# Kernel tuning notes

Measured on AMD Instinct MI355X. Metric: run time of the kernel, lower is better.

## Reference

```python
import jax, jax.numpy as jnp
import numpy as np

B, L, DIM, H, HD = 1, 2048, 2048, 16, 128  # head_dim = DIM // H; RoPE pairs = HD // 2


def setup_inputs() -> dict:
    key = jax.random.key(0)
    ks = jax.random.split(key, 6)
    x = jax.random.normal(ks[0], (B, L, DIM), dtype=jnp.float32)
    pe = jax.random.normal(ks[1], (1, 1, L, HD // 2, 2, 2), dtype=jnp.float32)
    qkv_w = jax.random.normal(ks[2], (3 * DIM, DIM), dtype=jnp.float32) * 0.02
    q_scale = jnp.ones((HD,), dtype=jnp.float32)
    k_scale = jnp.ones((HD,), dtype=jnp.float32)
    proj_w = jax.random.normal(ks[3], (DIM, DIM), dtype=jnp.float32) * 0.02
    proj_b = jnp.zeros((DIM,), dtype=jnp.float32)
    return {"x": x, "pe": pe, "qkv_w": qkv_w, "q_scale": q_scale,
            "k_scale": k_scale, "proj_w": proj_w, "proj_b": proj_b}


def _rmsnorm(t, scale):
    # per-head-dim RMSNorm, eps=1e-6, computed in fp32 (inputs already fp32)
    rrms = jax.lax.rsqrt(jnp.mean(t * t, axis=-1, keepdims=True) + 1e-6)
    return t * rrms * scale


def _apply_rope(q, k, pe):
    def rot(t):
        t_ = t.reshape(*t.shape[:-1], -1, 1, 2)  # [B,H,L,HD/2,1,2]
        out = pe[..., 0] * t_[..., 0] + pe[..., 1] * t_[..., 1]  # [B,H,L,HD/2,2]
        return out.reshape(t.shape)
    return rot(q), rot(k)


def reference(x, pe, qkv_w, q_scale, k_scale, proj_w, proj_b):
    b, l, _ = x.shape
    qkv = jnp.einsum('bld,ed->ble', x, qkv_w)  # [B, L, 3*DIM]
    qkv = qkv.reshape(b, l, 3, H, HD)
    # 'B L (K H D) -> K B H L D'
    qkv = jnp.transpose(qkv, (2, 0, 3, 1, 4))
    q, k, v = qkv[0], qkv[1], qkv[2]  # each [B, H, L, HD]
    q = _rmsnorm(q, q_scale)
    k = _rmsnorm(k, k_scale)
    q, k = _apply_rope(q, k, pe)
    scale = 1.0 / jnp.sqrt(jnp.asarray(HD, dtype=q.dtype))
    scores = jnp.einsum('bhqd,bhkd->bhqk', q, k) * scale
    attn = jax.nn.softmax(scores, axis=-1)
    out = jnp.einsum('bhqk,bhkd->bhqd', attn, v)  # [B, H, L, HD]
    out = jnp.transpose(out, (0, 2, 1, 3)).reshape(b, l, H * HD)  # 'B H L D -> B L (H D)'
    return jnp.einsum('bld,ed->ble', out, proj_w) + proj_b
```

## Files before the change

kernel.cpp:

```cpp
#include <hip/hip_runtime.h>
#include <hip/hip_bf16.h>
#include <math.h>

#define L_SEQ 2048
#define DIM   2048
#define NH    16
#define HD    128
#define TDIM  6144

typedef __attribute__((ext_vector_type(8))) short short8;
typedef __attribute__((ext_vector_type(4))) float f32x4;
typedef __attribute__((ext_vector_type(16))) float f32x16;
typedef __attribute__((ext_vector_type(4))) unsigned int u32x4;

__device__ __forceinline__ void gl_lds16(const void* g, void* l) {
  __builtin_amdgcn_global_load_lds(
      (const __attribute__((address_space(1))) unsigned int*)g,
      (__attribute__((address_space(3))) unsigned int*)l, 16, 0, 0);
}

__device__ __forceinline__ short bf16bits(float x) {
  __hip_bfloat16 h = __float2bfloat16(x);
  return *(short*)&h;
}

__device__ __forceinline__ float bits2f(short s) {
  unsigned int u = ((unsigned int)(unsigned short)s) << 16;
  return __uint_as_float(u);
}

__device__ __forceinline__ unsigned int pack_bf16(float a, float b) {
  __hip_bfloat162 h = __float22bfloat162_rn(make_float2(a, b));
  return *(unsigned int*)&h;
}

__global__ __launch_bounds__(256)
void cast2_bf16(const float* __restrict__ a, __hip_bfloat16* __restrict__ oa,
                const float* __restrict__ b, __hip_bfloat16* __restrict__ ob) {
  int i = (blockIdx.x * 256 + threadIdx.x) * 8;
  const float* src;
  __hip_bfloat16* dst;
  int off;
  if (i < DIM * DIM) { src = a; dst = oa; off = i; }
  else               { src = b; dst = ob; off = i - DIM * DIM; }
  float4 v0 = *(const float4*)(src + off);
  float4 v1 = *(const float4*)(src + off + 4);
  short8 o;
  o[0] = bf16bits(v0.x); o[1] = bf16bits(v0.y); o[2] = bf16bits(v0.z); o[3] = bf16bits(v0.w);
  o[4] = bf16bits(v1.x); o[5] = bf16bits(v1.y); o[6] = bf16bits(v1.z); o[7] = bf16bits(v1.w);
  *(short8*)(dst + off) = o;
}

__global__ __launch_bounds__(256)
void cast_bf16(const float* __restrict__ in, __hip_bfloat16* __restrict__ out, int n) {
  int i = (blockIdx.x * 256 + threadIdx.x) * 8;
  if (i >= n) return;
  float4 a = *(const float4*)(in + i);
  float4 b = *(const float4*)(in + i + 4);
  short8 o;
  o[0] = bf16bits(a.x); o[1] = bf16bits(a.y); o[2] = bf16bits(a.z); o[3] = bf16bits(a.w);
  o[4] = bf16bits(b.x); o[5] = bf16bits(b.y); o[6] = bf16bits(b.z); o[7] = bf16bits(b.w);
  *(short8*)(out + i) = o;
}

#define QKV_N 6144
#define QKV_K 2048

__global__ __launch_bounds__(512, 2)
void gemm_qkv_256(const __hip_bfloat16* __restrict__ A,
                  const __hip_bfloat16* __restrict__ B,
                  __hip_bfloat16* __restrict__ C) {
  extern __shared__ char smem[];
  const int tid  = threadIdx.x;
  const int lane = tid & 63, w = tid >> 6;
  const int l15  = lane & 15, quad = lane >> 4;
  const int wm   = w >> 2, wn = w & 3;

  const int orig = blockIdx.x;
  const int by = orig & 7;
  const int bx = orig >> 3;
  const int m0 = by * 256, n0 = bx * 256;

  const int ar0 = tid >> 2,         aq0 = tid & 3;
  const int ar1 = (512 + tid) >> 2, aq1 = (512 + tid) & 3;
  const __hip_bfloat16* pA0 = A + (size_t)(m0 + ar0) * QKV_K + aq0 * 8;
  const __hip_bfloat16* pA1 = A + (size_t)(m0 + ar1) * QKV_K + aq1 * 8;
  const __hip_bfloat16* pB0 = B + (size_t)(n0 + ar0) * QKV_K + aq0 * 8;
  const __hip_bfloat16* pB1 = B + (size_t)(n0 + ar1) * QKV_K + aq1 * 8;
  const int dst0 = w * 1024;

  f32x4 acc[8][4];
#pragma unroll
  for (int mi = 0; mi < 8; ++mi)
#pragma unroll
    for (int ni = 0; ni < 4; ++ni) acc[mi][ni] = (f32x4){0.f, 0.f, 0.f, 0.f};

  const int aoff = ((wm * 128 + l15) * 32 + quad * 8) * 2;
  const int boff = ((wn * 64 + l15) * 32 + quad * 8) * 2;

#pragma unroll
  for (int p = 0; p < 3; ++p) {
    char* Sp = smem + p * 32768;
    gl_lds16(pA0 + p * 32, Sp + dst0);
    gl_lds16(pA1 + p * 32, Sp + dst0 + 8192);
    gl_lds16(pB0 + p * 32, Sp + 16384 + dst0);
    gl_lds16(pB1 + p * 32, Sp + 16384 + dst0 + 8192);
  }
  asm volatile("s_waitcnt vmcnt(8)\n\ts_barrier" ::: "memory");

  for (int tb = 0; tb < 64; tb += 4) {
#pragma unroll
    for (int u = 0; u < 4; ++u) {
      const int t  = tb + u;
      const char* As = smem + u * 32768;
      const char* Bs = As + 16384;
      const int tn = (t + 3) & 63;
      char* Sn = smem + ((u + 3) & 3) * 32768;

      short8 a[8];
#pragma unroll
      for (int mi = 0; mi < 8; ++mi)
        a[mi] = *(const short8*)(As + aoff + mi * 1024);
      short8 b0 = *(const short8*)(Bs + boff);
      short8 b1 = *(const short8*)(Bs + boff + 1024);
      gl_lds16(pA0 + tn * 32, Sn + dst0);
      gl_lds16(pA1 + tn * 32, Sn + dst0 + 8192);
      __builtin_amdgcn_s_barrier();
      __builtin_amdgcn_s_setprio(1);
#pragma unroll
      for (int mi = 0; mi < 8; ++mi) {
        acc[mi][0] = __builtin_amdgcn_mfma_f32_16x16x32_bf16(a[mi], b0, acc[mi][0], 0, 0, 0);
        acc[mi][1] = __builtin_amdgcn_mfma_f32_16x16x32_bf16(a[mi], b1, acc[mi][1], 0, 0, 0);
      }
      __builtin_amdgcn_s_setprio(0);
      __builtin_amdgcn_s_barrier();

      short8 b2 = *(const short8*)(Bs + boff + 2048);
      short8 b3 = *(const short8*)(Bs + boff + 3072);
      gl_lds16(pB0 + tn * 32, Sn + 16384 + dst0);
      gl_lds16(pB1 + tn * 32, Sn + 16384 + dst0 + 8192);
      asm volatile("s_waitcnt vmcnt(8)\n\ts_barrier" ::: "memory");
      __builtin_amdgcn_s_setprio(1);
#pragma unroll
      for (int mi = 0; mi < 8; ++mi) {
        acc[mi][2] = __builtin_amdgcn_mfma_f32_16x16x32_bf16(a[mi], b2, acc[mi][2], 0, 0, 0);
        acc[mi][3] = __builtin_amdgcn_mfma_f32_16x16x32_bf16(a[mi], b3, acc[mi][3], 0, 0, 0);
      }
      __builtin_amdgcn_s_setprio(0);
      __builtin_amdgcn_s_barrier();
    }
  }

  const int crow = m0 + wm * 128 + quad * 4;
  const int ccol = n0 + wn * 64 + l15;
#pragma unroll
  for (int mi = 0; mi < 8; ++mi)
#pragma unroll
    for (int ni = 0; ni < 4; ++ni)
#pragma unroll
      for (int r = 0; r < 4; ++r)
        C[(size_t)(crow + mi * 16 + r) * QKV_N + ccol + ni * 16] =
            __float2bfloat16(acc[mi][ni][r]);
}

__global__ __launch_bounds__(256)
void qkv_epilogue(const __hip_bfloat16* __restrict__ C,
                  const float* __restrict__ q_scale, const float* __restrict__ k_scale,
                  const float* __restrict__ pe,
                  __hip_bfloat16* __restrict__ Qb, __hip_bfloat16* __restrict__ Kb,
                  __hip_bfloat16* __restrict__ Vt) {
  const int bid = blockIdx.x;
  const int t = threadIdx.x;
  if (bid < 512) {
    const int sec = bid >> 8;
    const int h   = (bid >> 4) & 15;
    const int rb  = bid & 15;
    const float* scale = sec ? k_scale : q_scale;
    const float qmul = sec ? 1.0f : 0.08838834764831845f;
    __hip_bfloat16* dst = sec ? Kb : Qb;

    const int row = t >> 1, half = t & 1;
    const int l = rb * 128 + row;
    const __hip_bfloat16* grow = C + (size_t)l * TDIM + sec * DIM + h * HD + half * 64;

    float ss = 0.f;
#pragma unroll
    for (int c8 = 0; c8 < 64; c8 += 8) {
      short8 v8 = *(const short8*)(grow + c8);
#pragma unroll
      for (int j = 0; j < 8; ++j) { float f = bits2f(v8[j]); ss += f * f; }
    }
    ss += __shfl_xor(ss, 1);
    const float rrms = rsqrtf(ss * (1.f / 128.f) + 1e-6f);

    const float* perow = pe + (size_t)l * 256 + half * 128;
    __hip_bfloat16* drow = dst + ((size_t)h * L_SEQ + l) * HD + half * 64;

#pragma unroll
    for (int c8 = 0; c8 < 64; c8 += 8) {
      short8 v8 = *(const short8*)(grow + c8);
      float f[8];
#pragma unroll
      for (int j = 0; j < 8; ++j)
        f[j] = bits2f(v8[j]) * rrms * scale[half * 64 + c8 + j];
      short8 o;
#pragma unroll
      for (int p = 0; p < 4; ++p) {
        float4 pp = *(const float4*)(perow + c8 * 2 + p * 4);
        float e = f[2 * p], od = f[2 * p + 1];
        o[2 * p]     = bf16bits((pp.x * e + pp.y * od) * qmul);
        o[2 * p + 1] = bf16bits((pp.z * e + pp.w * od) * qmul);
      }
      *(short8*)(drow + c8) = o;
    }
  } else {
    __shared__ short Tt[128 * 72];
    const int vb = bid - 512;
    const int h = vb >> 5, lb = vb & 31;
    const int l0 = lb * 64;
#pragma unroll
    for (int k = 0; k < 4; ++k) {
      int idx = t + k * 256;
      int row = idx >> 4, c = idx & 15;
      short8 v = *(const short8*)(C + (size_t)(l0 + row) * TDIM + 2 * DIM + h * HD + c * 8);
#pragma unroll
      for (int j = 0; j < 8; ++j) Tt[(c * 8 + j) * 72 + row] = v[j];
    }
    __syncthreads();
    const int d = t >> 1, lh = t & 1;
    __hip_bfloat16* vrow = Vt + ((size_t)h * HD + d) * L_SEQ + l0 + lh * 32;
#pragma unroll
    for (int k = 0; k < 4; ++k) {
      short8 o = *(const short8*)&Tt[d * 72 + lh * 32 + k * 8];
      *(short8*)(vrow + k * 8) = o;
    }
  }
}

__global__ __launch_bounds__(256)
void gemm_proj(const __hip_bfloat16* __restrict__ A, const __hip_bfloat16* __restrict__ B,
               const float* __restrict__ bias, float* __restrict__ C,
               int M, int N, int K) {
  const int n0 = blockIdx.x * 128, m0 = blockIdx.y * 128;
  const int t = threadIdx.x, lane = t & 63, w = t >> 6;
  const int l15 = lane & 15, quad = lane >> 4;
  const int wm = (w & 1) * 64, wn = (w >> 1) * 64;

  __shared__ __align__(16) __hip_bfloat16 As[128 * 32];
  __shared__ __align__(16) __hip_bfloat16 Bs[128 * 32];

  f32x4 acc[4][4];
#pragma unroll
  for (int mt = 0; mt < 4; ++mt)
#pragma unroll
    for (int nt = 0; nt < 4; ++nt) acc[mt][nt] = (f32x4){0.f, 0.f, 0.f, 0.f};

  const int arow  = lane >> 2;
  const int acol8 = (lane & 3) * 8;
  const __hip_bfloat16* Ab = A + (size_t)(m0 + w * 16 + arow) * K + acol8;
  const __hip_bfloat16* Bb = B + (size_t)(n0 + w * 16 + arow) * K + acol8;
  __hip_bfloat16* As_base = As + (size_t)(w * 16) * 32;
  __hip_bfloat16* Bs_base = Bs + (size_t)(w * 16) * 32;

  for (int kb = 0; kb < K; kb += 32) {
    gl_lds16(Ab + kb,                As_base);
    gl_lds16(Ab + kb + (size_t)64*K, As_base + 64 * 32);
    gl_lds16(Bb + kb,                Bs_base);
    gl_lds16(Bb + kb + (size_t)64*K, Bs_base + 64 * 32);
    __syncthreads();

    short8 am[4], bn[4];
#pragma unroll
    for (int mt = 0; mt < 4; ++mt)
      am[mt] = *(const short8*)&As[(size_t)(wm + mt*16 + l15) * 32 + quad * 8];
#pragma unroll
    for (int nt = 0; nt < 4; ++nt)
      bn[nt] = *(const short8*)&Bs[(size_t)(wn + nt*16 + l15) * 32 + quad * 8];
#pragma unroll
    for (int mt = 0; mt < 4; ++mt)
#pragma unroll
      for (int nt = 0; nt < 4; ++nt)
        acc[mt][nt] = __builtin_amdgcn_mfma_f32_16x16x32_bf16(am[mt], bn[nt], acc[mt][nt], 0, 0, 0);
    __syncthreads();
  }

#pragma unroll
  for (int mt = 0; mt < 4; ++mt)
#pragma unroll
    for (int nt = 0; nt < 4; ++nt) {
      int col = n0 + wn + nt * 16 + l15;
#pragma unroll
      for (int r = 0; r < 4; ++r) {
        int row = m0 + wm + mt * 16 + quad * 4 + r;
        C[(size_t)row * N + col] = acc[mt][nt][r] + bias[col];
      }
    }
}

#define NZ 4
#define ZLEN (L_SEQ / NZ)

__global__ __launch_bounds__(256, 3)
void attn_mfma(const __hip_bfloat16* __restrict__ Qb,
               const __hip_bfloat16* __restrict__ Kb,
               const __hip_bfloat16* __restrict__ Vt,
               __hip_bfloat16* __restrict__ Opart, float2* __restrict__ ml) {
  const int orig = blockIdx.x;
  const int wg   = (orig & 7) * 128 + (orig >> 3);
  const int h    = wg >> 6;
  const int rem  = wg & 63;
  const int z    = rem >> 4;
  const int q0   = (rem & 15) * 128;
  const int t    = threadIdx.x;
  const int lane = t & 63, w = t >> 6;
  const int l31  = lane & 31;
  const int u    = lane >> 5;

  __shared__ __align__(16) __hip_bfloat16 Ks[64 * 128];
  __shared__ __align__(16) __hip_bfloat16 Vs[128 * 64];

  const __hip_bfloat16* kbase = Kb + (size_t)h * L_SEQ * HD;
  const __hip_bfloat16* vbase = Vt + (size_t)h * HD * L_SEQ;

  short8 aq[8];
  {
    const __hip_bfloat16* qb = Qb + ((size_t)h * L_SEQ + q0 + w * 32 + l31) * HD + u * 8;
#pragma unroll
    for (int hh = 0; hh < 8; ++hh)
      aq[hh] = *(const short8*)(qb + hh * 16);
  }

  f32x16 o[4];
#pragma unroll
  for (int dt = 0; dt < 4; ++dt)
#pragma unroll
    for (int r = 0; r < 16; ++r) o[dt][r] = 0.f;
  float m_run = -1e30f, l_run = 0.f;

  for (int kt = 0; kt < ZLEN / 64; ++kt) {
    const int k0 = z * ZLEN + kt * 64;
#pragma unroll
    for (int i = 0; i < 4; ++i) {
      int krow = w * 16 + i * 4 + (lane >> 4);
      int kch  = (lane & 15) ^ (krow & 7);
      gl_lds16(kbase + (size_t)(k0 + krow) * HD + kch * 8,
               &Ks[(w * 16 + i * 4) * 128]);
    }
#pragma unroll
    for (int i = 0; i < 4; ++i) {
      int vrow = w * 32 + i * 8 + (lane >> 3);
      int vch  = (lane & 7) ^ (vrow & 7);
      gl_lds16(vbase + (size_t)vrow * L_SEQ + k0 + vch * 8,
               &Vs[(w * 32 + i * 8) * 64]);
    }
    __syncthreads();

#pragma unroll
    for (int ks = 0; ks < 2; ++ks) {
      const int krow = ks * 32 + l31;
      const char* krowp = (const char*)Ks + krow * 256;
      const int ksw = krow & 7;
      f32x16 s;
#pragma unroll
      for (int r = 0; r < 16; ++r) s[r] = 0.f;
      __builtin_amdgcn_s_setprio(1);
#pragma unroll
      for (int hh = 0; hh < 8; ++hh) {
        short8 ak = *(const short8*)(krowp + ((hh * 2 + u) ^ ksw) * 16);
        s = __builtin_amdgcn_mfma_f32_32x32x16_bf16(ak, aq[hh], s, 0, 0, 0);
      }
      __builtin_amdgcn_s_setprio(0);

      float rm = s[0];
#pragma unroll
      for (int r = 1; r < 16; ++r) rm = fmaxf(rm, s[r]);
      rm = fmaxf(rm, __shfl_xor(rm, 32));

      if (!__all(rm <= m_run + 8.f)) {
        float mnew = fmaxf(m_run, rm);
        float alpha = __expf(m_run - mnew);
        m_run = mnew;
        l_run *= alpha;
#pragma unroll
        for (int dt = 0; dt < 4; ++dt)
#pragma unroll
          for (int r = 0; r < 16; ++r) o[dt][r] *= alpha;
      }

      float sum = 0.f;
#pragma unroll
      for (int r = 0; r < 16; ++r) {
        float p = __expf(s[r] - m_run);
        s[r] = p;
        sum += p;
      }
      sum += __shfl_xor(sum, 32);
      l_run += sum;

      unsigned int W0 = pack_bf16(s[0],  s[1]),  W1 = pack_bf16(s[2],  s[3]);
      unsigned int W2 = pack_bf16(s[4],  s[5]),  W3 = pack_bf16(s[6],  s[7]);
      unsigned int W4 = pack_bf16(s[8],  s[9]),  W5 = pack_bf16(s[10], s[11]);
      unsigned int W6 = pack_bf16(s[12], s[13]), W7 = pack_bf16(s[14], s[15]);
      asm("v_permlane32_swap_b32 %0, %1" : "+v"(W0), "+v"(W2));
      asm("v_permlane32_swap_b32 %0, %1" : "+v"(W1), "+v"(W3));
      asm("v_permlane32_swap_b32 %0, %1" : "+v"(W4), "+v"(W6));
      asm("v_permlane32_swap_b32 %0, %1" : "+v"(W5), "+v"(W7));
      u32x4 pb0 = {W0, W1, W2, W3};
      u32x4 pb1 = {W4, W5, W6, W7};
      short8 ap0 = *(short8*)&pb0;
      short8 ap1 = *(short8*)&pb1;

      __builtin_amdgcn_s_setprio(1);
#pragma unroll
      for (int dt = 0; dt < 4; ++dt) {
        const int d = dt * 32 + l31;
        const char* vrowp = (const char*)Vs + d * 128;
        const int vsw = d & 7;
        short8 av0 = *(const short8*)(vrowp + ((ks * 4 + u) ^ vsw) * 16);
        o[dt] = __builtin_amdgcn_mfma_f32_32x32x16_bf16(av0, ap0, o[dt], 0, 0, 0);
        short8 av1 = *(const short8*)(vrowp + ((ks * 4 + 2 + u) ^ vsw) * 16);
        o[dt] = __builtin_amdgcn_mfma_f32_32x32x16_bf16(av1, ap1, o[dt], 0, 0, 0);
      }
      __builtin_amdgcn_s_setprio(0);
    }
    __syncthreads();
  }

  const float linv = 1.f / l_run;
  char* Ot = (char*)Ks + w * 8192;
  const int qsw = l31 & 7;
#pragma unroll
  for (int dt = 0; dt < 4; ++dt)
#pragma unroll
    for (int p = 0; p < 8; ++p) {
      unsigned int v = pack_bf16(o[dt][2 * p] * linv, o[dt][2 * p + 1] * linv);
      int dpair = dt * 16 + (p & 1) + (p >> 1) * 4 + 2 * u;
      *(unsigned int*)(Ot + l31 * 256 + ((dpair >> 2) ^ qsw) * 16 + (dpair & 3) * 4) = v;
    }
  __syncthreads();
  {
    const int qr = lane >> 1, half = lane & 1;
    const char* Orow = (char*)Ks + w * 8192 + qr * 256;
    __hip_bfloat16* gout =
        Opart + ((size_t)(z * NH + h) * L_SEQ + q0 + w * 32 + qr) * HD;
#pragma unroll
    for (int c8 = 0; c8 < 8; ++c8) {
      int chunk = half * 8 + c8;
      short8 v = *(const short8*)(Orow + ((chunk ^ (qr & 7)) * 16));
      *(short8*)(gout + chunk * 8) = v;
    }
  }
  if (lane < 32) {
    size_t rb = (size_t)(z * NH + h) * L_SEQ + q0 + w * 32;
    ml[rb + l31] = make_float2(m_run, l_run);
  }
}

__global__ __launch_bounds__(256)
void attn_combine4(const __hip_bfloat16* __restrict__ Opart,
                   const float2* __restrict__ ml,
                   __hip_bfloat16* __restrict__ out) {
  const int h  = blockIdx.y;
  const int q  = blockIdx.x * 16 + (threadIdx.x >> 4);
  const int d8 = (threadIdx.x & 15) * 8;
  size_t idx[NZ];
  float2 a[NZ];
#pragma unroll
  for (int zz = 0; zz < NZ; ++zz) {
    idx[zz] = ((size_t)zz * NH + h) * L_SEQ + q;
    a[zz] = ml[idx[zz]];
  }
  float M = fmaxf(fmaxf(a[0].x, a[1].x), fmaxf(a[2].x, a[3].x));
  float wz[NZ];
  float tot = 0.f;
#pragma unroll
  for (int zz = 0; zz < NZ; ++zz) {
    wz[zz] = __expf(a[zz].x - M) * a[zz].y;
    tot += wz[zz];
  }
  float inv = 1.f / tot;
  float acc[8] = {0.f, 0.f, 0.f, 0.f, 0.f, 0.f, 0.f, 0.f};
#pragma unroll
  for (int zz = 0; zz < NZ; ++zz) {
    short8 ov = *(const short8*)&Opart[idx[zz] * HD + d8];
#pragma unroll
    for (int j = 0; j < 8; ++j) acc[j] += wz[zz] * bits2f(ov[j]);
  }
  short8 r;
#pragma unroll
  for (int j = 0; j < 8; ++j) r[j] = bf16bits(acc[j] * inv);
  *(short8*)&out[(size_t)q * DIM + h * HD + d8] = r;
}

extern "C" void kernel_launch(void* const* d_in, const int* in_sizes, int n_in,
                              void* d_out, int out_size, void* d_ws, size_t ws_size,
                              hipStream_t stream) {
  const float* x       = (const float*)d_in[0];
  const float* pe      = (const float*)d_in[1];
  const float* qkv_w   = (const float*)d_in[2];
  const float* q_scale = (const float*)d_in[3];
  const float* k_scale = (const float*)d_in[4];
  const float* proj_w  = (const float*)d_in[5];
  const float* proj_b  = (const float*)d_in[6];
  float* out = (float*)d_out;

  char* base = (char*)d_ws;
  __hip_bfloat16* xb       = (__hip_bfloat16*)base;
  __hip_bfloat16* wb       = (__hip_bfloat16*)(base + 8388608);
  __hip_bfloat16* Cq       = (__hip_bfloat16*)(base + 33554432);
  __hip_bfloat16* Qb       = (__hip_bfloat16*)base;
  __hip_bfloat16* Kb       = (__hip_bfloat16*)(base + 8388608);
  __hip_bfloat16* Vt       = (__hip_bfloat16*)(base + 16777216);
  __hip_bfloat16* Opart    = (__hip_bfloat16*)(base + 33554432);
  float2*         ml       = (float2*)(base + 25165824);
  __hip_bfloat16* attn_out = (__hip_bfloat16*)base;
  __hip_bfloat16* pwb      = (__hip_bfloat16*)(base + 33554432);

  static bool attr_done = false;
  if (!attr_done) {
    hipFuncSetAttribute((const void*)gemm_qkv_256,
                        hipFuncAttributeMaxDynamicSharedMemorySize, 131072);
    attr_done = true;
  }

  cast2_bf16<<<dim3((DIM * DIM + TDIM * DIM) / (256 * 8)), 256, 0, stream>>>(
      x, xb, qkv_w, wb);

  gemm_qkv_256<<<dim3((TDIM / 256) * (L_SEQ / 256)), 512, 131072, stream>>>(xb, wb, Cq);

  qkv_epilogue<<<dim3(1024), 256, 0, stream>>>(Cq, q_scale, k_scale, pe, Qb, Kb, Vt);

  attn_mfma<<<dim3(NZ * NH * (L_SEQ / 128)), 256, 0, stream>>>(Qb, Kb, Vt, Opart, ml);

  attn_combine4<<<dim3(L_SEQ / 16, NH), 256, 0, stream>>>(Opart, ml, attn_out);

  cast_bf16<<<dim3(DIM * DIM / (256 * 8)), 256, 0, stream>>>(proj_w, pwb, DIM * DIM);

  gemm_proj<<<dim3(DIM / 128, DIM / 128), 256, 0, stream>>>(
      attn_out, pwb, proj_b, out, L_SEQ, DIM, DIM);
}
```

Measured before the change: 318.6 us.

## Pipeline proj GEMM with 4-stage LDS ring, swizzle LDS, remap QKV tiles

Replaces the simple single-buffered projection GEMM with a 4-stage global_load_lds ring buffer. Its compute is split into two MFMA halves separated by barriers, with setprio and an XOR swizzle of LDS columns. The QKV GEMM gets the same LDS swizzle plus a block-to-tile remap that groups tiles per XCD for L2 locality. The goal is to hide global load latency, cut LDS bank conflicts and improve cache reuse, at the cost of more complex barrier choreography.

```diff
diff --git a/kernel.cpp b/kernel.cpp
--- a/kernel.cpp
+++ b/kernel.cpp
@@ -77,12 +77,14 @@
   const int wm   = w >> 2, wn = w & 3;
 
   const int orig = blockIdx.x;
-  const int by = orig & 7;
-  const int bx = orig >> 3;
+  const int c   = orig & 7;
+  const int idx = orig >> 3;
+  const int by  = (c & 1) * 4 + idx / 6;
+  const int bx  = (c >> 1) * 6 + idx % 6;
   const int m0 = by * 256, n0 = bx * 256;
 
-  const int ar0 = tid >> 2,         aq0 = tid & 3;
-  const int ar1 = (512 + tid) >> 2, aq1 = (512 + tid) & 3;
+  const int ar0 = tid >> 2,         aq0 = (tid & 3) ^ ((ar0 >> 1) & 3);
+  const int ar1 = (512 + tid) >> 2, aq1 = (tid & 3) ^ ((ar1 >> 1) & 3);
   const __hip_bfloat16* pA0 = A + (size_t)(m0 + ar0) * QKV_K + aq0 * 8;
   const __hip_bfloat16* pA1 = A + (size_t)(m0 + ar1) * QKV_K + aq1 * 8;
   const __hip_bfloat16* pB0 = B + (size_t)(n0 + ar0) * QKV_K + aq0 * 8;
@@ -95,8 +97,9 @@
 #pragma unroll
     for (int ni = 0; ni < 4; ++ni) acc[mi][ni] = (f32x4){0.f, 0.f, 0.f, 0.f};
 
-  const int aoff = ((wm * 128 + l15) * 32 + quad * 8) * 2;
-  const int boff = ((wn * 64 + l15) * 32 + quad * 8) * 2;
+  const int sq   = (l15 >> 1) & 3;
+  const int aoff = ((wm * 128 + l15) * 32 + (quad ^ sq) * 8) * 2;
+  const int boff = ((wn * 64 + l15) * 32 + (quad ^ sq) * 8) * 2;
 
 #pragma unroll
   for (int p = 0; p < 3; ++p) {
@@ -237,63 +240,108 @@
   }
 }
 
-__global__ __launch_bounds__(256)
-void gemm_proj(const __hip_bfloat16* __restrict__ A, const __hip_bfloat16* __restrict__ B,
-               const float* __restrict__ bias, float* __restrict__ C,
-               int M, int N, int K) {
-  const int n0 = blockIdx.x * 128, m0 = blockIdx.y * 128;
-  const int t = threadIdx.x, lane = t & 63, w = t >> 6;
-  const int l15 = lane & 15, quad = lane >> 4;
-  const int wm = (w & 1) * 64, wn = (w >> 1) * 64;
-
-  __shared__ __align__(16) __hip_bfloat16 As[128 * 32];
-  __shared__ __align__(16) __hip_bfloat16 Bs[128 * 32];
+#define PJ_N 2048
+#define PJ_K 2048
+
+__global__ __launch_bounds__(256, 2)
+void gemm_proj_128(const __hip_bfloat16* __restrict__ A,
+                   const __hip_bfloat16* __restrict__ B,
+                   const float* __restrict__ bias, float* __restrict__ C) {
+  __shared__ __align__(16) char smem[65536];
+  const int tid  = threadIdx.x;
+  const int lane = tid & 63, w = tid >> 6;
+  const int l15  = lane & 15, quad = lane >> 4;
+  const int wm   = (w >> 1) * 64, wn = (w & 1) * 64;
+
+  const int orig = blockIdx.x;
+  const int c   = orig & 7;
+  const int idx = orig >> 3;
+  const int by  = (c >> 1) * 4 + (idx & 3);
+  const int bx  = (c & 1) * 8 + (idx >> 2);
+  const int m0 = by * 128, n0 = bx * 128;
+
+  const int ar0 = tid >> 2,         aq0 = (tid & 3) ^ ((ar0 >> 1) & 3);
+  const int ar1 = (256 + tid) >> 2, aq1 = (tid & 3) ^ ((ar1 >> 1) & 3);
+  const __hip_bfloat16* pA0 = A + (size_t)(m0 + ar0) * PJ_K + aq0 * 8;
+  const __hip_bfloat16* pA1 = A + (size_t)(m0 + ar1) * PJ_K + aq1 * 8;
+  const __hip_bfloat16* pB0 = B + (size_t)(n0 + ar0) * PJ_K + aq0 * 8;
+  const __hip_bfloat16* pB1 = B + (size_t)(n0 + ar1) * PJ_K + aq1 * 8;
+  const int dst0 = w * 1024;
 
   f32x4 acc[4][4];
 #pragma unroll
-  for (int mt = 0; mt < 4; ++mt)
-#pragma unroll
-    for (int nt = 0; nt < 4; ++nt) acc[mt][nt] = (f32x4){0.f, 0.f, 0.f, 0.f};
-
-  const int arow  = lane >> 2;
-  const int acol8 = (lane & 3) * 8;
-  const __hip_bfloat16* Ab = A + (size_t)(m0 + w * 16 + arow) * K + acol8;
-  const __hip_bfloat16* Bb = B + (size_t)(n0 + w * 16 + arow) * K + acol8;
-  __hip_bfloat16* As_base = As + (size_t)(w * 16) * 32;
-  __hip_bfloat16* Bs_base = Bs + (size_t)(w * 16) * 32;
-
-  for (int kb = 0; kb < K; kb += 32) {
-    gl_lds16(Ab + kb,                As_base);
-    gl_lds16(Ab + kb + (size_t)64*K, As_base + 64 * 32);
-    gl_lds16(Bb + kb,                Bs_base);
-    gl_lds16(Bb + kb + (size_t)64*K, Bs_base + 64 * 32);
-    __syncthreads();
-
-    short8 am[4], bn[4];
-#pragma unroll
-    for (int mt = 0; mt < 4; ++mt)
-      am[mt] = *(const short8*)&As[(size_t)(wm + mt*16 + l15) * 32 + quad * 8];
-#pragma unroll
-    for (int nt = 0; nt < 4; ++nt)
-      bn[nt] = *(const short8*)&Bs[(size_t)(wn + nt*16 + l15) * 32 + quad * 8];
-#pragma unroll
-    for (int mt = 0; mt < 4; ++mt)
-#pragma unroll
-      for (int nt = 0; nt < 4; ++nt)
-        acc[mt][nt] = __builtin_amdgcn_mfma_f32_16x16x32_bf16(am[mt], bn[nt], acc[mt][nt], 0, 0, 0);
-    __syncthreads();
-  }
-
-#pragma unroll
-  for (int mt = 0; mt < 4; ++mt)
-#pragma unroll
-    for (int nt = 0; nt < 4; ++nt) {
-      int col = n0 + wn + nt * 16 + l15;
-#pragma unroll
-      for (int r = 0; r < 4; ++r) {
-        int row = m0 + wm + mt * 16 + quad * 4 + r;
-        C[(size_t)row * N + col] = acc[mt][nt][r] + bias[col];
-      }
+  for (int mi = 0; mi < 4; ++mi)
+#pragma unroll
+    for (int ni = 0; ni < 4; ++ni) acc[mi][ni] = (f32x4){0.f, 0.f, 0.f, 0.f};
+
+  const int sq   = (l15 >> 1) & 3;
+  const int aoff = ((wm + l15) * 32 + (quad ^ sq) * 8) * 2;
+  const int boff = 8192 + ((wn + l15) * 32 + (quad ^ sq) * 8) * 2;
+
+#pragma unroll
+  for (int p = 0; p < 3; ++p) {
+    char* Sp = smem + p * 16384;
+    gl_lds16(pA0 + p * 32, Sp + dst0);
+    gl_lds16(pA1 + p * 32, Sp + dst0 + 4096);
+    gl_lds16(pB0 + p * 32, Sp + 8192 + dst0);
+    gl_lds16(pB1 + p * 32, Sp + 8192 + dst0 + 4096);
+  }
+  asm volatile("s_waitcnt vmcnt(8)\n\ts_barrier" ::: "memory");
+
+  for (int tb = 0; tb < 64; tb += 4) {
+#pragma unroll
+    for (int u = 0; u < 4; ++u) {
+      const int t  = tb + u;
+      const char* As = smem + u * 16384;
+      const char* Bs = As;
+      const int tn = (t + 3) & 63;
+      char* Sn = smem + ((u + 3) & 3) * 16384;
+
+      short8 a[4];
+#pragma unroll
+      for (int mi = 0; mi < 4; ++mi)
+        a[mi] = *(const short8*)(As + aoff + mi * 1024);
+      short8 b0 = *(const short8*)(Bs + boff);
+      short8 b1 = *(const short8*)(Bs + boff + 1024);
+      gl_lds16(pA0 + tn * 32, Sn + dst0);
+      gl_lds16(pA1 + tn * 32, Sn + dst0 + 4096);
+      __builtin_amdgcn_s_barrier();
+      __builtin_amdgcn_s_setprio(1);
+#pragma unroll
+      for (int mi = 0; mi < 4; ++mi) {
+        acc[mi][0] = __builtin_amdgcn_mfma_f32_16x16x32_bf16(a[mi], b0, acc[mi][0], 0, 0, 0);
+        acc[mi][1] = __builtin_amdgcn_mfma_f32_16x16x32_bf16(a[mi], b1, acc[mi][1], 0, 0, 0);
+      }
+      __builtin_amdgcn_s_setprio(0);
+      __builtin_amdgcn_s_barrier();
+
+      short8 b2 = *(const short8*)(Bs + boff + 2048);
+      short8 b3 = *(const short8*)(Bs + boff + 3072);
+      gl_lds16(pB0 + tn * 32, Sn + 8192 + dst0);
+      gl_lds16(pB1 + tn * 32, Sn + 8192 + dst0 + 4096);
+      asm volatile("s_waitcnt vmcnt(8)\n\ts_barrier" ::: "memory");
+      __builtin_amdgcn_s_setprio(1);
+#pragma unroll
+      for (int mi = 0; mi < 4; ++mi) {
+        acc[mi][2] = __builtin_amdgcn_mfma_f32_16x16x32_bf16(a[mi], b2, acc[mi][2], 0, 0, 0);
+        acc[mi][3] = __builtin_amdgcn_mfma_f32_16x16x32_bf16(a[mi], b3, acc[mi][3], 0, 0, 0);
+      }
+      __builtin_amdgcn_s_setprio(0);
+      __builtin_amdgcn_s_barrier();
+    }
+  }
+
+  const int crow = m0 + wm + quad * 4;
+  const int ccol = n0 + wn + l15;
+#pragma unroll
+  for (int mi = 0; mi < 4; ++mi)
+#pragma unroll
+    for (int ni = 0; ni < 4; ++ni) {
+      float bv = bias[ccol + ni * 16];
+#pragma unroll
+      for (int r = 0; r < 4; ++r)
+        C[(size_t)(crow + mi * 16 + r) * PJ_N + ccol + ni * 16] =
+            acc[mi][ni][r] + bv;
     }
 }
 
@@ -536,6 +584,5 @@
 
   cast_bf16<<<dim3(DIM * DIM / (256 * 8)), 256, 0, stream>>>(proj_w, pwb, DIM * DIM);
 
-  gemm_proj<<<dim3(DIM / 128, DIM / 128), 256, 0, stream>>>(
-      attn_out, pwb, proj_b, out, L_SEQ, DIM, DIM);
-}
+  gemm_proj_128<<<dim3(256), 256, 0, stream>>>(attn_out, pwb, proj_b, out);
+}
```

After: 288.7 us. -9.4%, faster.
